# Optimization experiments

Hardware: AMD Instinct MI355X
Metric: run time of the kernel (lower is better)

## Reference

```python
import jax, jax.numpy as jnp
import numpy as np

N_NODES = 50000
N_EDGES = 640000
D = 128      # in_feats
OUT = 128    # out_feats


def setup_inputs() -> dict:
    key = jax.random.key(0)
    ks = jax.random.split(key, 8)
    feat = jax.random.normal(ks[0], (N_NODES, D), dtype=jnp.float32)
    weight = jax.random.uniform(ks[1], (N_EDGES,), dtype=jnp.float32)
    src = jax.random.randint(ks[2], (N_EDGES,), 0, N_NODES, dtype=jnp.int64)
    dst = jax.random.randint(ks[3], (N_EDGES,), 0, N_NODES, dtype=jnp.int64)
    # xavier_uniform with relu gain ~ sqrt(2)*sqrt(6/(fan_in+fan_out))
    g = np.sqrt(2.0)
    lim_pool = g * np.sqrt(6.0 / (D + D))
    lim_neigh = g * np.sqrt(6.0 / (2 * D + OUT))
    W_pool = jax.random.uniform(ks[4], (D, D), dtype=jnp.float32, minval=-lim_pool, maxval=lim_pool)
    b_pool = jnp.zeros((D,), dtype=jnp.float32)
    W_neigh = jax.random.uniform(ks[5], (OUT, 2 * D), dtype=jnp.float32, minval=-lim_neigh, maxval=lim_neigh)
    b_neigh = jnp.zeros((OUT,), dtype=jnp.float32)
    return {"feat": feat, "weight": weight, "src": src, "dst": dst,
            "W_pool": W_pool, "b_pool": b_pool, "W_neigh": W_neigh, "b_neigh": b_neigh}


def reference(feat, weight, src, dst, W_pool, b_pool, W_neigh, b_neigh):
    n = feat.shape[0]
    # fc_pool: h = feat @ W_pool.T + b_pool  -> [N, D]
    h = feat @ W_pool.T + b_pool
    # u_mul_e: per-edge message m_e = h[src_e] * w_e  -> [E, D]
    m = h[src] * weight[:, None]
    # max reduce over incoming edges (scatter-max by dst)
    neigh = jax.ops.segment_max(m, dst, num_segments=n)
    # zero-degree nodes get 0 (segment_max fills empties with -inf)
    deg = jax.ops.segment_sum(jnp.ones_like(weight), dst, num_segments=n)
    neigh = jnp.where(deg[:, None] > 0, neigh, jnp.zeros((), dtype=feat.dtype))
    # fc_neigh on concat(feat, neigh)
    rst = jnp.concatenate([feat, neigh], axis=1) @ W_neigh.T + b_neigh
    return rst
```

## Files before the change

### kernel.cpp

```cpp
#include <hip/hip_runtime.h>
#include <cstdint>
#include <cstddef>

#define N_NODES 50000
#define N_EDGES 640000
#define DF 128

#define NBUCK 196
#define BCAP  6144
#define ECAP  8192
#define PA_BLOCKS 250
#define DUMMY_ROW 50000

typedef __attribute__((ext_vector_type(8))) short bf16x8;
typedef __attribute__((ext_vector_type(4))) float f32x4;

__device__ inline unsigned short f2bf(float f) {
    unsigned int u = __float_as_uint(f);
    return (unsigned short)((u + 0x7fffu + ((u >> 16) & 1u)) >> 16);
}

#define NF4 (N_NODES * DF / 4)
#define NWG (3 * 2048)
__global__ __launch_bounds__(256) void k1_setup_bucket(
    const float* __restrict__ feat,
    const float* __restrict__ W_pool,
    const float* __restrict__ W_neigh,
    const int* __restrict__ src,
    const int* __restrict__ dst,
    const float* __restrict__ w,
    unsigned short* __restrict__ featb,
    unsigned short* __restrict__ hb,
    unsigned short* __restrict__ Wp_f,
    unsigned short* __restrict__ Wn1_f,
    unsigned short* __restrict__ Wn2_f,
    int* __restrict__ bucketcnt,
    uint2* __restrict__ staging)
{
    int bid = blockIdx.x;
    int t = threadIdx.x;
    if (bid < PA_BLOCKS) {
        __shared__ int cnt[NBUCK];
        __shared__ int runbase[NBUCK];
        int base = bid * 2560;
        if (t < NBUCK) cnt[t] = 0;
        __syncthreads();
        uint2 rec[10];
        int bk[10];
        #pragma unroll
        for (int i = 0; i < 10; ++i) {
            int e = base + i * 256 + t;
            int s = src[e], d = dst[e];
            bk[i] = d >> 8;
            rec[i].x = (unsigned int)s | ((unsigned int)(d & 255) << 16);
            rec[i].y = __float_as_uint(w[e]);
            atomicAdd(&cnt[bk[i]], 1);
        }
        __syncthreads();
        if (t < NBUCK) {
            runbase[t] = atomicAdd(&bucketcnt[t], cnt[t]);
            cnt[t] = 0;
        }
        __syncthreads();
        #pragma unroll
        for (int i = 0; i < 10; ++i) {
            int r = atomicAdd(&cnt[bk[i]], 1);
            int pos = runbase[bk[i]] + r;
            if (pos < BCAP) staging[bk[i] * BCAP + pos] = rec[i];
        }
    } else if (bid < 250 + NF4 / 256) {
        int idx = (bid - PA_BLOCKS) * 256 + t;
        float4 v = ((const float4*)feat)[idx];
        ushort4 o;
        o.x = f2bf(v.x); o.y = f2bf(v.y); o.z = f2bf(v.z); o.w = f2bf(v.w);
        ((ushort4*)featb)[idx] = o;
    } else if (bid < 250 + NF4 / 256 + NWG / 256) {
        int g = (bid - PA_BLOCKS - NF4 / 256) * 256 + t;
        int m = g >> 11;
        int r8 = g & 2047;
        int L = r8 & 63, tt = (r8 >> 6) & 3, c = r8 >> 8;
        int o = c * 16 + (L & 15);
        int kb = tt * 32 + (L >> 4) * 8;
        const float* srcp;
        unsigned short* dstp;
        if (m == 0)      { srcp = W_pool  + o * 128 + kb;       dstp = Wp_f;  }
        else if (m == 1) { srcp = W_neigh + o * 256 + kb;       dstp = Wn1_f; }
        else             { srcp = W_neigh + o * 256 + 128 + kb; dstp = Wn2_f; }
        ushort4 lo, hi;
        float4 a = ((const float4*)srcp)[0];
        float4 b = ((const float4*)srcp)[1];
        lo.x = f2bf(a.x); lo.y = f2bf(a.y); lo.z = f2bf(a.z); lo.w = f2bf(a.w);
        hi.x = f2bf(b.x); hi.y = f2bf(b.y); hi.z = f2bf(b.z); hi.w = f2bf(b.w);
        ((ushort4*)(dstp + r8 * 8))[0] = lo;
        ((ushort4*)(dstp + r8 * 8))[1] = hi;
    } else {
        if (t < DF) hb[(size_t)DUMMY_ROW * DF + t] = 0xFF7Fu;
    }
}

#define GEMMB 196
__global__ __launch_bounds__(1024) void k2_gemm_passb(
    const unsigned short* __restrict__ featb,
    const unsigned short* __restrict__ Wp_f,
    const float* __restrict__ b_pool,
    unsigned short* __restrict__ hb,
    const int* __restrict__ bucketcnt,
    const uint2* __restrict__ staging,
    int* __restrict__ offsets,
    int* __restrict__ nend,
    uint2* __restrict__ edges)
{
    int t = threadIdx.x;
    if (blockIdx.x < GEMMB) {
        int wave = blockIdx.x * 16 + (t >> 6);
        int lane = t & 63;
        int m0 = wave * 16;
        if (m0 >= N_NODES) return;
        const int n = lane & 15, quad = lane >> 4;

        f32x4 acc[8];
        #pragma unroll
        for (int c = 0; c < 8; ++c) {
            float bv = b_pool[c * 16 + n];
            acc[c] = (f32x4){bv, bv, bv, bv};
        }
        const unsigned short* aptr = featb + (size_t)(m0 + n) * DF + quad * 8;
        #pragma unroll
        for (int tt = 0; tt < 4; ++tt) {
            bf16x8 af = *(const bf16x8*)(aptr + tt * 32);
            #pragma unroll
            for (int c = 0; c < 8; ++c) {
                bf16x8 bf = *(const bf16x8*)(Wp_f + (size_t)((c * 4 + tt) * 64 + lane) * 8);
                acc[c] = __builtin_amdgcn_mfma_f32_16x16x32_bf16(af, bf, acc[c], 0, 0, 0);
            }
        }
        #pragma unroll
        for (int c = 0; c < 8; ++c)
            #pragma unroll
            for (int r = 0; r < 4; ++r)
                hb[(size_t)(m0 + quad * 4 + r) * DF + c * 16 + n] = f2bf(acc[c][r]);
    } else {
        __shared__ int dcnt[256];
        __shared__ int sc[256];
        int b = blockIdx.x - GEMMB;
        int cnt = bucketcnt[b];
        if (cnt > BCAP) cnt = BCAP;

        if (t < 256) dcnt[t] = 0;
        __syncthreads();

        uint2 rec[6];
        int nit = (cnt + 1023) >> 10;
        for (int i = 0; i < nit; ++i) {
            int idx = i * 1024 + t;
            if (idx < cnt) {
                rec[i] = staging[(size_t)b * BCAP + idx];
                atomicAdd(&dcnt[(rec[i].x >> 16) & 255], 1);
            }
        }
        __syncthreads();
        int mydeg = 0, mypad = 0;
        if (t < 256) {
            mydeg = dcnt[t];
            mypad = (mydeg + 7) & ~7;
            sc[t] = mypad;
        }
        __syncthreads();
        #pragma unroll
        for (int off = 1; off < 256; off <<= 1) {
            int u = (t < 256 && t >= off) ? sc[t - off] : 0;
            __syncthreads();
            if (t < 256) sc[t] += u;
            __syncthreads();
        }
        if (t < 256) {
            int beg = b * ECAP + sc[t] - mypad;
            int node = b * 256 + t;
            if (node < N_NODES) {
                offsets[node] = beg;
                nend[node] = beg + mypad;
            }
            dcnt[t] = beg;
            uint2 dmy; dmy.x = DUMMY_ROW; dmy.y = 0x3F800000u;
            for (int k = mydeg; k < mypad; ++k) edges[beg + k] = dmy;
        }
        __syncthreads();
        for (int i = 0; i < nit; ++i) {
            int idx = i * 1024 + t;
            if (idx < cnt) {
                int dl = (rec[i].x >> 16) & 255;
                int pos = atomicAdd(&dcnt[dl], 1);
                uint2 fin;
                fin.x = rec[i].x & 0xFFFFu;
                fin.y = rec[i].y;
                edges[pos] = fin;
            }
        }
    }
}

__global__ __launch_bounds__(256) void neigh_max_kernel(
    const unsigned short* __restrict__ hb, const int* __restrict__ offsets,
    const int* __restrict__ nend,
    const uint2* __restrict__ edges,
    unsigned short* __restrict__ neighb)
{
    int gwave = (blockIdx.x * 256 + threadIdx.x) >> 6;
    if (gwave >= N_NODES) return;
    int node = __builtin_amdgcn_readfirstlane(gwave);
    int lane = threadIdx.x & 63;
    const int half = lane >> 5;
    const int q = lane & 31;

    int beg = offsets[node], end = nend[node];
    float4 acc = make_float4(-3.4e38f, -3.4e38f, -3.4e38f, -3.4e38f);

    for (int e = beg; e < end; e += 8) {
        uint2 e0 = edges[e],     e1 = edges[e + 1], e2 = edges[e + 2], e3 = edges[e + 3];
        uint2 e4 = edges[e + 4], e5 = edges[e + 5], e6 = edges[e + 6], e7 = edges[e + 7];
        uint2 mA = half ? e1 : e0;
        uint2 mB = half ? e3 : e2;
        uint2 mC = half ? e5 : e4;
        uint2 mD = half ? e7 : e6;
        float wA = __uint_as_float(mA.y);
        float wB = __uint_as_float(mB.y);
        float wC = __uint_as_float(mC.y);
        float wD = __uint_as_float(mD.y);
        uint2 pA = *(const uint2*)(hb + (size_t)mA.x * DF + q * 4);
        uint2 pB = *(const uint2*)(hb + (size_t)mB.x * DF + q * 4);
        uint2 pC = *(const uint2*)(hb + (size_t)mC.x * DF + q * 4);
        uint2 pD = *(const uint2*)(hb + (size_t)mD.x * DF + q * 4);
        acc.x = fmaxf(acc.x, __uint_as_float(pA.x << 16)          * wA);
        acc.y = fmaxf(acc.y, __uint_as_float(pA.x & 0xffff0000u)  * wA);
        acc.z = fmaxf(acc.z, __uint_as_float(pA.y << 16)          * wA);
        acc.w = fmaxf(acc.w, __uint_as_float(pA.y & 0xffff0000u)  * wA);
        acc.x = fmaxf(acc.x, __uint_as_float(pB.x << 16)          * wB);
        acc.y = fmaxf(acc.y, __uint_as_float(pB.x & 0xffff0000u)  * wB);
        acc.z = fmaxf(acc.z, __uint_as_float(pB.y << 16)          * wB);
        acc.w = fmaxf(acc.w, __uint_as_float(pB.y & 0xffff0000u)  * wB);
        acc.x = fmaxf(acc.x, __uint_as_float(pC.x << 16)          * wC);
        acc.y = fmaxf(acc.y, __uint_as_float(pC.x & 0xffff0000u)  * wC);
        acc.z = fmaxf(acc.z, __uint_as_float(pC.y << 16)          * wC);
        acc.w = fmaxf(acc.w, __uint_as_float(pC.y & 0xffff0000u)  * wC);
        acc.x = fmaxf(acc.x, __uint_as_float(pD.x << 16)          * wD);
        acc.y = fmaxf(acc.y, __uint_as_float(pD.x & 0xffff0000u)  * wD);
        acc.z = fmaxf(acc.z, __uint_as_float(pD.y << 16)          * wD);
        acc.w = fmaxf(acc.w, __uint_as_float(pD.y & 0xffff0000u)  * wD);
    }

    float4 o;
    o.x = fmaxf(acc.x, __shfl_xor(acc.x, 32));
    o.y = fmaxf(acc.y, __shfl_xor(acc.y, 32));
    o.z = fmaxf(acc.z, __shfl_xor(acc.z, 32));
    o.w = fmaxf(acc.w, __shfl_xor(acc.w, 32));
    if (beg == end) o = make_float4(0.f, 0.f, 0.f, 0.f);
    if (half == 0) {
        ushort4 ob;
        ob.x = f2bf(o.x); ob.y = f2bf(o.y); ob.z = f2bf(o.z); ob.w = f2bf(o.w);
        *(ushort4*)(neighb + (size_t)node * DF + q * 4) = ob;
    }
}

__global__ __launch_bounds__(256) void gemm_out(
    const unsigned short* __restrict__ featb,
    const unsigned short* __restrict__ neighb,
    const unsigned short* __restrict__ Wn1_f,
    const unsigned short* __restrict__ Wn2_f,
    const float* __restrict__ bias,
    float* __restrict__ out)
{
    int wave = (blockIdx.x * 256 + threadIdx.x) >> 6;
    int lane = threadIdx.x & 63;
    int m0 = wave * 16;
    if (m0 >= N_NODES) return;
    const int n = lane & 15, quad = lane >> 4;

    f32x4 acc[8];
    #pragma unroll
    for (int c = 0; c < 8; ++c) {
        float bv = bias[c * 16 + n];
        acc[c] = (f32x4){bv, bv, bv, bv};
    }

    const unsigned short* a0 = featb  + (size_t)(m0 + n) * DF + quad * 8;
    const unsigned short* a1 = neighb + (size_t)(m0 + n) * DF + quad * 8;
    #pragma unroll
    for (int t = 0; t < 4; ++t) {
        bf16x8 af = *(const bf16x8*)(a0 + t * 32);
        #pragma unroll
        for (int c = 0; c < 8; ++c) {
            bf16x8 bf = *(const bf16x8*)(Wn1_f + (size_t)((c * 4 + t) * 64 + lane) * 8);
            acc[c] = __builtin_amdgcn_mfma_f32_16x16x32_bf16(af, bf, acc[c], 0, 0, 0);
        }
    }
    #pragma unroll
    for (int t = 0; t < 4; ++t) {
        bf16x8 af = *(const bf16x8*)(a1 + t * 32);
        #pragma unroll
        for (int c = 0; c < 8; ++c) {
            bf16x8 bf = *(const bf16x8*)(Wn2_f + (size_t)((c * 4 + t) * 64 + lane) * 8);
            acc[c] = __builtin_amdgcn_mfma_f32_16x16x32_bf16(af, bf, acc[c], 0, 0, 0);
        }
    }

    #pragma unroll
    for (int c = 0; c < 8; ++c)
        #pragma unroll
        for (int r = 0; r < 4; ++r)
            out[(size_t)(m0 + quad * 4 + r) * DF + c * 16 + n] = acc[c][r];
}

extern "C" void kernel_launch(void* const* d_in, const int* in_sizes, int n_in,
                              void* d_out, int out_size, void* d_ws, size_t ws_size,
                              hipStream_t stream) {
    const float* feat    = (const float*)d_in[0];
    const float* weight  = (const float*)d_in[1];
    const int*   src     = (const int*)d_in[2];
    const int*   dst     = (const int*)d_in[3];
    const float* W_pool  = (const float*)d_in[4];
    const float* b_pool  = (const float*)d_in[5];
    const float* W_neigh = (const float*)d_in[6];
    const float* b_neigh = (const float*)d_in[7];
    float* out = (float*)d_out;

    char* ws = (char*)d_ws;
    unsigned short* featb  = (unsigned short*)(ws);
    unsigned short* hb     = (unsigned short*)(ws + 12800000);
    unsigned short* Wp_f   = (unsigned short*)(ws + 25600512);
    unsigned short* Wn1_f  = (unsigned short*)(ws + 25633280);
    unsigned short* Wn2_f  = (unsigned short*)(ws + 25666048);
    int*   offsets   = (int*)  (ws + 25698816);
    int*   nend      = (int*)  (ws + 25898816);
    int*   bucketcnt = (int*)  (ws + 26098816);
    uint2* staging   = (uint2*)(ws + 26099840);
    uint2* edges     = (uint2*)(ws + 35733632);
    unsigned short* neighb = (unsigned short*)(ws + 48578688);

    hipMemsetAsync(bucketcnt, 0, 1024, stream);

    const int K1_BLOCKS = PA_BLOCKS + NF4 / 256 + NWG / 256 + 1;
    k1_setup_bucket<<<K1_BLOCKS, 256, 0, stream>>>(
        feat, W_pool, W_neigh, src, dst, weight,
        featb, hb, Wp_f, Wn1_f, Wn2_f, bucketcnt, staging);

    k2_gemm_passb<<<GEMMB + NBUCK, 1024, 0, stream>>>(
        featb, Wp_f, b_pool, hb, bucketcnt, staging, offsets, nend, edges);

    neigh_max_kernel<<<(N_NODES + 3) / 4, 256, 0, stream>>>(
        hb, offsets, nend, edges, neighb);

    gemm_out<<<782, 256, 0, stream>>>(
        featb, neighb, Wn1_f, Wn2_f, b_neigh, out);
}
```

Before: 162.3 us.

## Shrink dst buckets to 64 nodes and use 256-thread blocks for GEMM and pass B

Dst buckets now cover 64 nodes instead of 256, giving 782 buckets with smaller capacities. Pass B drops to 256-thread blocks and replaces the shared-memory prefix scan with a wave-level shuffle scan. The pool GEMM also uses 256-thread blocks (782 of them) to match. The aim is more and smaller blocks for better GPU occupancy and fewer block-wide syncs. In exchange, pass A does more global atomics on bucket counters, and the per-bucket capacity (BCAP 1280) is tighter, so overflow would silently drop edges.

```diff
diff --git a/kernel.cpp b/kernel.cpp
--- a/kernel.cpp
+++ b/kernel.cpp
@@ -6,10 +6,11 @@
 #define N_EDGES 640000
 #define DF 128
 
-#define NBUCK 196
-#define BCAP  6144
-#define ECAP  8192
+#define NBUCK 782
+#define BCAP  1280
+#define ECAP  1536
 #define PA_BLOCKS 250
+#define GEMMB 782
 #define DUMMY_ROW 50000
 
 typedef __attribute__((ext_vector_type(8))) short bf16x8;
@@ -22,7 +23,7 @@
 
 #define NF4 (N_NODES * DF / 4)
 #define NWG (3 * 2048)
-__global__ __launch_bounds__(256) void k1_setup_bucket(
+__global__ __launch_bounds__(256) void k1_passa_featb_frags(
     const float* __restrict__ feat,
     const float* __restrict__ W_pool,
     const float* __restrict__ W_neigh,
@@ -43,7 +44,7 @@
         __shared__ int cnt[NBUCK];
         __shared__ int runbase[NBUCK];
         int base = bid * 2560;
-        if (t < NBUCK) cnt[t] = 0;
+        for (int i = t; i < NBUCK; i += 256) cnt[i] = 0;
         __syncthreads();
         uint2 rec[10];
         int bk[10];
@@ -51,22 +52,22 @@
         for (int i = 0; i < 10; ++i) {
             int e = base + i * 256 + t;
             int s = src[e], d = dst[e];
-            bk[i] = d >> 8;
-            rec[i].x = (unsigned int)s | ((unsigned int)(d & 255) << 16);
+            bk[i] = d >> 6;
+            rec[i].x = (unsigned int)s | ((unsigned int)(d & 63) << 16);
             rec[i].y = __float_as_uint(w[e]);
             atomicAdd(&cnt[bk[i]], 1);
         }
         __syncthreads();
-        if (t < NBUCK) {
-            runbase[t] = atomicAdd(&bucketcnt[t], cnt[t]);
-            cnt[t] = 0;
+        for (int i = t; i < NBUCK; i += 256) {
+            runbase[i] = atomicAdd(&bucketcnt[i], cnt[i]);
+            cnt[i] = 0;
         }
         __syncthreads();
         #pragma unroll
         for (int i = 0; i < 10; ++i) {
             int r = atomicAdd(&cnt[bk[i]], 1);
             int pos = runbase[bk[i]] + r;
-            if (pos < BCAP) staging[bk[i] * BCAP + pos] = rec[i];
+            if (pos < BCAP) staging[(size_t)bk[i] * BCAP + pos] = rec[i];
         }
     } else if (bid < 250 + NF4 / 256) {
         int idx = (bid - PA_BLOCKS) * 256 + t;
@@ -98,8 +99,7 @@
     }
 }
 
-#define GEMMB 196
-__global__ __launch_bounds__(1024) void k2_gemm_passb(
+__global__ __launch_bounds__(256) void k2_gemm_passb(
     const unsigned short* __restrict__ featb,
     const unsigned short* __restrict__ Wp_f,
     const float* __restrict__ b_pool,
@@ -112,7 +112,7 @@
 {
     int t = threadIdx.x;
     if (blockIdx.x < GEMMB) {
-        int wave = blockIdx.x * 16 + (t >> 6);
+        int wave = blockIdx.x * 4 + (t >> 6);
         int lane = t & 63;
         int m0 = wave * 16;
         if (m0 >= N_NODES) return;
@@ -140,42 +140,35 @@
             for (int r = 0; r < 4; ++r)
                 hb[(size_t)(m0 + quad * 4 + r) * DF + c * 16 + n] = f2bf(acc[c][r]);
     } else {
-        __shared__ int dcnt[256];
-        __shared__ int sc[256];
+        __shared__ int dcnt[64];
         int b = blockIdx.x - GEMMB;
         int cnt = bucketcnt[b];
         if (cnt > BCAP) cnt = BCAP;
 
-        if (t < 256) dcnt[t] = 0;
-        __syncthreads();
-
-        uint2 rec[6];
-        int nit = (cnt + 1023) >> 10;
+        if (t < 64) dcnt[t] = 0;
+        __syncthreads();
+
+        uint2 rec[5];
+        int nit = (cnt + 255) >> 8;
         for (int i = 0; i < nit; ++i) {
-            int idx = i * 1024 + t;
+            int idx = i * 256 + t;
             if (idx < cnt) {
                 rec[i] = staging[(size_t)b * BCAP + idx];
-                atomicAdd(&dcnt[(rec[i].x >> 16) & 255], 1);
-            }
-        }
-        __syncthreads();
-        int mydeg = 0, mypad = 0;
-        if (t < 256) {
-            mydeg = dcnt[t];
-            mypad = (mydeg + 7) & ~7;
-            sc[t] = mypad;
-        }
-        __syncthreads();
-        #pragma unroll
-        for (int off = 1; off < 256; off <<= 1) {
-            int u = (t < 256 && t >= off) ? sc[t - off] : 0;
-            __syncthreads();
-            if (t < 256) sc[t] += u;
-            __syncthreads();
-        }
-        if (t < 256) {
-            int beg = b * ECAP + sc[t] - mypad;
-            int node = b * 256 + t;
+                atomicAdd(&dcnt[(rec[i].x >> 16) & 63], 1);
+            }
+        }
+        __syncthreads();
+        if (t < 64) {
+            int mydeg = dcnt[t];
+            int mypad = (mydeg + 7) & ~7;
+            int v = mypad;
+            #pragma unroll
+            for (int off = 1; off < 64; off <<= 1) {
+                int u = __shfl_up(v, off, 64);
+                if (t >= off) v += u;
+            }
+            int beg = b * ECAP + v - mypad;
+            int node = b * 64 + t;
             if (node < N_NODES) {
                 offsets[node] = beg;
                 nend[node] = beg + mypad;
@@ -186,9 +179,9 @@
         }
         __syncthreads();
         for (int i = 0; i < nit; ++i) {
-            int idx = i * 1024 + t;
+            int idx = i * 256 + t;
             if (idx < cnt) {
-                int dl = (rec[i].x >> 16) & 255;
+                int dl = (rec[i].x >> 16) & 63;
                 int pos = atomicAdd(&dcnt[dl], 1);
                 uint2 fin;
                 fin.x = rec[i].x & 0xFFFFu;
@@ -332,18 +325,18 @@
     int*   offsets   = (int*)  (ws + 25698816);
     int*   nend      = (int*)  (ws + 25898816);
     int*   bucketcnt = (int*)  (ws + 26098816);
-    uint2* staging   = (uint2*)(ws + 26099840);
-    uint2* edges     = (uint2*)(ws + 35733632);
-    unsigned short* neighb = (unsigned short*)(ws + 48578688);
-
-    hipMemsetAsync(bucketcnt, 0, 1024, stream);
+    uint2* staging   = (uint2*)(ws + 26102016);
+    uint2* edges     = (uint2*)(ws + 34109696);
+    unsigned short* neighb = (unsigned short*)(ws + 43718912);
+
+    hipMemsetAsync(bucketcnt, 0, NBUCK * sizeof(int), stream);
 
     const int K1_BLOCKS = PA_BLOCKS + NF4 / 256 + NWG / 256 + 1;
-    k1_setup_bucket<<<K1_BLOCKS, 256, 0, stream>>>(
+    k1_passa_featb_frags<<<K1_BLOCKS, 256, 0, stream>>>(
         feat, W_pool, W_neigh, src, dst, weight,
         featb, hb, Wp_f, Wn1_f, Wn2_f, bucketcnt, staging);
 
-    k2_gemm_passb<<<GEMMB + NBUCK, 1024, 0, stream>>>(
+    k2_gemm_passb<<<GEMMB + NBUCK, 256, 0, stream>>>(
         featb, Wp_f, b_pool, hb, bucketcnt, staging, offsets, nend, edges);
 
     neigh_max_kernel<<<(N_NODES + 3) / 4, 256, 0, stream>>>(
```

Result: slower. 174.3 us (+7.4%).
